# Kernel tuning notes

Hardware: AMD Instinct MI355X
Metric: run time of the kernel (lower is better)

The kernel has to match this reference:

```python
import jax, jax.numpy as jnp
import numpy as np

BATCH, N, FIN, FOUT = 131072, 16, 32, 32
NEG = -9.0e15


def setup_inputs() -> dict:
    key = jax.random.key(0)
    ks = jax.random.split(key, 8)
    stdv = 1.0 / np.sqrt(FOUT)
    return {
        "x": jax.random.normal(ks[0], (BATCH, N, FIN), dtype=jnp.float32),
        "basis": jax.random.normal(ks[1], (N, N), dtype=jnp.float32) * 0.25,
        "adj": jax.random.uniform(ks[2], (N, N), dtype=jnp.float32),  # all > 0 -> dense mask
        "e": jax.random.uniform(ks[3], (N, N), dtype=jnp.float32),    # edge weights at mask positions
        "W_e": jax.random.normal(ks[4], (FOUT * 10, FIN * 10), dtype=jnp.float32) * 0.02,
        "W_2": jax.random.normal(ks[5], (FOUT * 3, FIN * 3), dtype=jnp.float32) * 0.05,
        "W_3": jax.random.normal(ks[6], (FOUT * 3, FIN * 3), dtype=jnp.float32) * 0.05,
        "bias": jax.random.uniform(ks[7], (FOUT,), dtype=jnp.float32, minval=-stdv, maxval=stdv),
    }


def reference(x, basis, adj, e, W_e, W_2, W_3, bias):
    # x: [B, n, Fin]; basis: [n, n]
    Bsz = x.shape[0]
    # input.permute(2,0,1) @ B, then permute(1,0,2) -> [B, Fin, n]
    x_irrep = jnp.einsum('bnf,nm->bfm', x, basis)
    # three basis-block linears (torch F.linear: y = x @ W.T)
    out_e = (x_irrep[:, :, :10].reshape(Bsz, -1) @ W_e.T).reshape(Bsz, FOUT, 10)
    out_2 = (x_irrep[:, :, 10:13].reshape(Bsz, -1) @ W_2.T).reshape(Bsz, FOUT, 3)
    out_3 = (x_irrep[:, :, 13:].reshape(Bsz, -1) @ W_3.T).reshape(Bsz, FOUT, 3)
    out_irrep = jnp.concatenate([out_e, out_2, out_3], axis=2)  # [B, Fout, n]
    # (out_irrep @ B.T) then permute(0,2,1) -> [B, n, Fout]
    h = jnp.einsum('bon,mn->bmo', out_irrep, basis)
    # masked softmax adjacency; output = (softmax(adj) * I) @ h == diag-scale of h
    logits = jnp.where(adj > 0, e, NEG)
    adj_sm = jax.nn.softmax(logits, axis=1)
    diag = jnp.diagonal(adj_sm)  # [n]
    return h * diag[None, :, None] + bias[None, None, :]
```

## Files before the change

### kernel.cpp

```cpp
#include <hip/hip_runtime.h>
#include <hip/hip_bf16.h>

typedef __attribute__((ext_vector_type(4))) float f32x4_t;
typedef __attribute__((ext_vector_type(8))) short bf16x8_t;

__device__ __forceinline__ short f2bfs(float x) {
    union { __hip_bfloat16 h; short s; } u;
    u.h = __float2bfloat16(x);
    return u.s;
}

__device__ __forceinline__ void gload_lds16(const float* g, float* l) {
    __builtin_amdgcn_global_load_lds(
        (const __attribute__((address_space(1))) void*)g,
        (__attribute__((address_space(3))) void*)l, 16, 0, 0);
}

__global__ void build_M_kernel(const float* __restrict__ basis,
                               const float* __restrict__ adj,
                               const float* __restrict__ e,
                               const float* __restrict__ We,
                               const float* __restrict__ W2,
                               const float* __restrict__ W3,
                               unsigned short* __restrict__ Mfrag) {
    const int t = blockIdx.x * blockDim.x + threadIdx.x;
    const int c = t >> 9;
    const int k = t & 511;
    const int m  = c >> 5, o = c & 31;
    const int n2 = k >> 5, f = k & 31;

    float lv[16];
    float mx = -3.4e38f;
#pragma unroll
    for (int j = 0; j < 16; ++j) {
        float a = adj[m * 16 + j];
        float v = (a > 0.0f) ? e[m * 16 + j] : -9.0e15f;
        lv[j] = v;
        mx = fmaxf(mx, v);
    }
    float s = 0.0f;
#pragma unroll
    for (int j = 0; j < 16; ++j) s += expf(lv[j] - mx);
    const float dg = expf(lv[m] - mx) / s;

    float acc = 0.0f;
#pragma unroll
    for (int n = 0; n < 10; ++n) {
        float t2 = 0.0f;
#pragma unroll
        for (int m2 = 0; m2 < 10; ++m2)
            t2 += We[(o * 10 + n) * 320 + f * 10 + m2] * basis[n2 * 16 + m2];
        acc += basis[m * 16 + n] * t2;
    }
#pragma unroll
    for (int n = 0; n < 3; ++n) {
        float t2 = 0.0f;
#pragma unroll
        for (int m2 = 0; m2 < 3; ++m2)
            t2 += W2[(o * 3 + n) * 96 + f * 3 + m2] * basis[n2 * 16 + 10 + m2];
        acc += basis[m * 16 + 10 + n] * t2;
    }
#pragma unroll
    for (int n = 0; n < 3; ++n) {
        float t2 = 0.0f;
#pragma unroll
        for (int m2 = 0; m2 < 3; ++m2)
            t2 += W3[(o * 3 + n) * 96 + f * 3 + m2] * basis[n2 * 16 + 13 + m2];
        acc += basis[m * 16 + 13 + n] * t2;
    }

    const float Mv = dg * acc;

    const int ks = k >> 5;
    const int g  = (k >> 3) & 3;
    const int j  = k & 7;
    const int idx = ((ks * 32 + (c >> 4)) * 64 + ((c & 15) + 16 * g)) * 8 + j;
    Mfrag[idx] = (unsigned short)f2bfs(Mv);
}

__global__ __launch_bounds__(512, 4)
void gemm_kernel(const float* __restrict__ X,
                 const unsigned short* __restrict__ Mfrag,
                 const float* __restrict__ bias,
                 float* __restrict__ Y) {
    __shared__ float lds[16384];

    const int tid  = threadIdx.x;
    const int lane = tid & 63;
    const int wave = tid >> 6;
    const int l15  = lane & 15;
    const int g    = lane >> 4;
    const size_t rowbase = (size_t)blockIdx.x * 64;

    const int colbase = wave * 64;
    const unsigned short* bp = Mfrag + ((size_t)((colbase >> 4) * 64) + lane) * 8;

    f32x4_t acc[4][4];
#pragma unroll
    for (int a = 0; a < 4; ++a)
#pragma unroll
        for (int b = 0; b < 4; ++b)
            acc[a][b] = (f32x4_t){0.f, 0.f, 0.f, 0.f};

    auto stage = [&](int q, int b) {
        float* dstbase = &lds[b * 8192];
        const float* xq = X + rowbase * 512 + q * 128;
#pragma unroll
        for (int i = 0; i < 4; ++i) {
            const int p   = wave * 4 + i;
            const int row = p * 2 + (lane >> 5);
            const int ul  = (lane & 31) ^ (row & 7);
            gload_lds16(xq + (size_t)row * 512 + ul * 4, dstbase + p * 256);
        }
    };

    auto compute = [&](int q, int b) {
        const float* buf = &lds[b * 8192];
        const int s = l15 & 7;
#pragma unroll
        for (int ksl = 0; ksl < 4; ++ksl) {
            const int ks = q * 4 + ksl;
            bf16x8_t bfrag[4];
#pragma unroll
            for (int ni = 0; ni < 4; ++ni)
                bfrag[ni] = *reinterpret_cast<const bf16x8_t*>(bp + (size_t)ks * 16384 + ni * 512);
            bf16x8_t afrag[4];
#pragma unroll
            for (int mi = 0; mi < 4; ++mi) {
                const int row  = mi * 16 + l15;
                const int ulo  = (ksl * 8 + g * 2) ^ s;
                const int uhi  = (ksl * 8 + g * 2 + 1) ^ s;
                f32x4_t lo = *reinterpret_cast<const f32x4_t*>(&buf[row * 128 + ulo * 4]);
                f32x4_t hi = *reinterpret_cast<const f32x4_t*>(&buf[row * 128 + uhi * 4]);
#pragma unroll
                for (int j = 0; j < 4; ++j) {
                    afrag[mi][j]     = f2bfs(lo[j]);
                    afrag[mi][j + 4] = f2bfs(hi[j]);
                }
            }
#pragma unroll
            for (int mi = 0; mi < 4; ++mi)
#pragma unroll
                for (int ni = 0; ni < 4; ++ni)
                    acc[mi][ni] = __builtin_amdgcn_mfma_f32_16x16x32_bf16(
                        afrag[mi], bfrag[ni], acc[mi][ni], 0, 0, 0);
        }
    };

    stage(0, 0);
    __syncthreads();
    stage(1, 1);  compute(0, 0);  __syncthreads();
    stage(2, 0);  compute(1, 1);  __syncthreads();
    stage(3, 1);  compute(2, 0);  __syncthreads();
                  compute(3, 1);
    __syncthreads();

    constexpr int SW = 68;
    float* scr = &lds[wave * 1088];
    const float b_lo = bias[l15];
    const float b_hi = bias[16 + l15];

#pragma unroll
    for (int mi = 0; mi < 4; ++mi) {
#pragma unroll
        for (int ni = 0; ni < 4; ++ni) {
            const float bb = (ni & 1) ? b_hi : b_lo;
#pragma unroll
            for (int r = 0; r < 4; ++r)
                scr[(g * 4 + r) * SW + ni * 16 + l15] = acc[mi][ni][r] + bb;
        }
#pragma unroll
        for (int it = 0; it < 4; ++it) {
            const int flat = it * 64 + lane;
            const int row  = flat >> 4;
            const int c4   = flat & 15;
            f32x4_t v = *reinterpret_cast<const f32x4_t*>(&scr[row * SW + c4 * 4]);
            float* yp = Y + (rowbase + mi * 16 + row) * 512 + colbase + c4 * 4;
            __builtin_nontemporal_store(v, reinterpret_cast<f32x4_t*>(yp));
        }
    }
}

extern "C" void kernel_launch(void* const* d_in, const int* in_sizes, int n_in,
                              void* d_out, int out_size, void* d_ws, size_t ws_size,
                              hipStream_t stream) {
    const float* x     = (const float*)d_in[0];
    const float* basis = (const float*)d_in[1];
    const float* adj   = (const float*)d_in[2];
    const float* e     = (const float*)d_in[3];
    const float* We    = (const float*)d_in[4];
    const float* W2    = (const float*)d_in[5];
    const float* W3    = (const float*)d_in[6];
    const float* bias  = (const float*)d_in[7];

    unsigned short* Mfrag = (unsigned short*)d_ws;
    if (ws_size < 512u * 512u * 2u) return;

    const int Bsz = in_sizes[0] / 512;
    build_M_kernel<<<512, 512, 0, stream>>>(basis, adj, e, We, W2, W3, Mfrag);
    gemm_kernel<<<Bsz / 64, 512, 0, stream>>>(x, Mfrag, bias, (float*)d_out);
}
```

Measured before the change: 150.6 us.

## Stage weight fragments through LDS with a triple-buffered 16-step K pipeline

The GEMM main loop now walks K in 16 steps of 32 with a triple-buffered LDS ring. Each step loads both a thin X slice and the matching bf16 weight fragments asynchronously via global_load_lds. Waits are explicit vmcnt counts plus a raw s_barrier instead of four large stages with __syncthreads. Weights used to be read straight from global memory by every wave of every block; now they are shared through LDS to cut redundant L2 traffic and hide latency with deeper prefetch. LDS use grows to about 120 KB and the occupancy hint is dropped, so fewer blocks fit per CU, and the hand-written vmcnt bookkeeping is fragile.

```diff
diff --git a/kernel.cpp b/kernel.cpp
--- a/kernel.cpp
+++ b/kernel.cpp
@@ -10,7 +10,7 @@
     return u.s;
 }
 
-__device__ __forceinline__ void gload_lds16(const float* g, float* l) {
+__device__ __forceinline__ void gload_lds16(const void* g, void* l) {
     __builtin_amdgcn_global_load_lds(
         (const __attribute__((address_space(1))) void*)g,
         (__attribute__((address_space(3))) void*)l, 16, 0, 0);
@@ -78,12 +78,14 @@
     Mfrag[idx] = (unsigned short)f2bfs(Mv);
 }
 
-__global__ __launch_bounds__(512, 4)
+__global__ __launch_bounds__(512)
 void gemm_kernel(const float* __restrict__ X,
                  const unsigned short* __restrict__ Mfrag,
                  const float* __restrict__ bias,
                  float* __restrict__ Y) {
-    __shared__ float lds[16384];
+    __shared__ float lds_f32[30720];
+    float* Abuf = lds_f32;
+    unsigned short* Bbuf = reinterpret_cast<unsigned short*>(lds_f32 + 6144);
 
     const int tid  = threadIdx.x;
     const int lane = tid & 63;
@@ -91,9 +93,23 @@
     const int l15  = lane & 15;
     const int g    = lane >> 4;
     const size_t rowbase = (size_t)blockIdx.x * 64;
-
     const int colbase = wave * 64;
-    const unsigned short* bp = Mfrag + ((size_t)((colbase >> 4) * 64) + lane) * 8;
+
+    const int arow = lane >> 3;
+    const int aunit = (lane & 7) ^ arow;
+    const float* asrc = X + (rowbase + wave * 8 + arow) * 512 + aunit * 4;
+    const unsigned short* bsrc = Mfrag + lane * 8;
+
+    auto stage = [&](int t) {
+        const int b = t % 3;
+        gload_lds16(asrc + t * 32, Abuf + b * 2048 + wave * 256);
+#pragma unroll
+        for (int i = 0; i < 4; ++i) {
+            const int f = wave * 4 + i;
+            gload_lds16(bsrc + (size_t)t * 16384 + f * 512,
+                        Bbuf + b * 16384 + f * 512);
+        }
+    };
 
     f32x4_t acc[4][4];
 #pragma unroll
@@ -102,61 +118,55 @@
         for (int b = 0; b < 4; ++b)
             acc[a][b] = (f32x4_t){0.f, 0.f, 0.f, 0.f};
 
-    auto stage = [&](int q, int b) {
-        float* dstbase = &lds[b * 8192];
-        const float* xq = X + rowbase * 512 + q * 128;
-#pragma unroll
-        for (int i = 0; i < 4; ++i) {
-            const int p   = wave * 4 + i;
-            const int row = p * 2 + (lane >> 5);
-            const int ul  = (lane & 31) ^ (row & 7);
-            gload_lds16(xq + (size_t)row * 512 + ul * 4, dstbase + p * 256);
-        }
-    };
-
-    auto compute = [&](int q, int b) {
-        const float* buf = &lds[b * 8192];
-        const int s = l15 & 7;
-#pragma unroll
-        for (int ksl = 0; ksl < 4; ++ksl) {
-            const int ks = q * 4 + ksl;
-            bf16x8_t bfrag[4];
+    const int s = l15 & 7;
+
+    stage(0);
+    stage(1);
+    asm volatile("s_waitcnt vmcnt(5)" ::: "memory");
+    asm volatile("s_barrier" ::: "memory");
+
+#pragma unroll
+    for (int t = 0; t < 16; ++t) {
+        if (t + 2 < 16) stage(t + 2);
+
+        const int b = t % 3;
+        const float* Ab = Abuf + b * 2048;
+        const unsigned short* Bb = Bbuf + b * 16384;
+
+        bf16x8_t bfr[4], afr[4];
+#pragma unroll
+        for (int ni = 0; ni < 4; ++ni)
+            bfr[ni] = *reinterpret_cast<const bf16x8_t*>(
+                Bb + ((colbase >> 4) + ni) * 512 + lane * 8);
+#pragma unroll
+        for (int mi = 0; mi < 4; ++mi) {
+            const int row = mi * 16 + l15;
+            f32x4_t lo = *reinterpret_cast<const f32x4_t*>(
+                Ab + row * 32 + ((g * 2) ^ s) * 4);
+            f32x4_t hi = *reinterpret_cast<const f32x4_t*>(
+                Ab + row * 32 + ((g * 2 + 1) ^ s) * 4);
+#pragma unroll
+            for (int j = 0; j < 4; ++j) {
+                afr[mi][j]     = f2bfs(lo[j]);
+                afr[mi][j + 4] = f2bfs(hi[j]);
+            }
+        }
+#pragma unroll
+        for (int mi = 0; mi < 4; ++mi)
 #pragma unroll
             for (int ni = 0; ni < 4; ++ni)
-                bfrag[ni] = *reinterpret_cast<const bf16x8_t*>(bp + (size_t)ks * 16384 + ni * 512);
-            bf16x8_t afrag[4];
-#pragma unroll
-            for (int mi = 0; mi < 4; ++mi) {
-                const int row  = mi * 16 + l15;
-                const int ulo  = (ksl * 8 + g * 2) ^ s;
-                const int uhi  = (ksl * 8 + g * 2 + 1) ^ s;
-                f32x4_t lo = *reinterpret_cast<const f32x4_t*>(&buf[row * 128 + ulo * 4]);
-                f32x4_t hi = *reinterpret_cast<const f32x4_t*>(&buf[row * 128 + uhi * 4]);
-#pragma unroll
-                for (int j = 0; j < 4; ++j) {
-                    afrag[mi][j]     = f2bfs(lo[j]);
-                    afrag[mi][j + 4] = f2bfs(hi[j]);
-                }
-            }
-#pragma unroll
-            for (int mi = 0; mi < 4; ++mi)
-#pragma unroll
-                for (int ni = 0; ni < 4; ++ni)
-                    acc[mi][ni] = __builtin_amdgcn_mfma_f32_16x16x32_bf16(
-                        afrag[mi], bfrag[ni], acc[mi][ni], 0, 0, 0);
-        }
-    };
-
-    stage(0, 0);
+                acc[mi][ni] = __builtin_amdgcn_mfma_f32_16x16x32_bf16(
+                    afr[mi], bfr[ni], acc[mi][ni], 0, 0, 0);
+
+        if (t < 14)       asm volatile("s_waitcnt vmcnt(5)" ::: "memory");
+        else if (t == 14) asm volatile("s_waitcnt vmcnt(0)" ::: "memory");
+        if (t < 15)       asm volatile("s_barrier" ::: "memory");
+    }
+
     __syncthreads();
-    stage(1, 1);  compute(0, 0);  __syncthreads();
-    stage(2, 0);  compute(1, 1);  __syncthreads();
-    stage(3, 1);  compute(2, 0);  __syncthreads();
-                  compute(3, 1);
-    __syncthreads();
 
     constexpr int SW = 68;
-    float* scr = &lds[wave * 1088];
+    float* scr = lds_f32 + 6144 + wave * (16 * SW);
     const float b_lo = bias[l15];
     const float b_hi = bias[16 + l15];
 
```

New measurement: 145.3 us. -3.5%, faster.
